# Optimization experiments

Hardware: AMD Instinct MI355X
Metric: run time of the kernel (lower is better)

Reference implementation:

```python
import jax, jax.numpy as jnp
import numpy as np

M, N, RANK = 4096, 4096, 64
LORA_ALPHA = 0.8
CODEBOOK_SCALE = 1.03  # E8P12 opt_scale; decompressed weights are divided by it


def fwht(x):
    """Normalized fast Walsh-Hadamard transform along the last axis (power-of-2 length).
    Matches matmul_hadU for power-of-2 dims (had_K is None, K=1)."""
    n = x.shape[-1]
    orig = x.shape
    x = x.reshape(-1, n)
    h = 1
    while h < n:
        x = x.reshape(-1, n // (2 * h), 2, h)
        a, b = x[:, :, 0, :], x[:, :, 1, :]
        x = jnp.stack([a + b, a - b], axis=2).reshape(-1, n)
        h *= 2
    return (x / jnp.sqrt(jnp.float32(n))).reshape(orig)


def decode_e8p(codes, grid):
    """E8P lattice codebook dequant (decompress_packed_e8p semantics).
    codes: int32 [M, N//8], one 16-bit codeword per 8-weight group.
    grid:  int32 [256] packed abs codebook; 8 nibbles per entry, nibble = 2*|w| in {1,3,5,7}.
    Bit layout: [0:8]=abs grid index, [8:15]=signs of first 7 coords,
    [15]=global +/-0.25 shift. 8th sign keeps the negative-sign count even."""
    abs_idx = codes & 0xFF
    sign_bits = (codes >> 8) & 0x7F
    shift_bit = (codes >> 15) & 1
    packed = grid[abs_idx]                                      # [M, N//8] int32
    nibs = (packed[..., None] >> (4 * jnp.arange(8))) & 0xF     # [M, N//8, 8]
    s7 = 1.0 - 2.0 * ((sign_bits[..., None] >> jnp.arange(7)) & 1).astype(jnp.float32)
    s8 = jnp.prod(s7, axis=-1, keepdims=True)                   # parity sign for 8th coord
    signs = jnp.concatenate([s7, s8], axis=-1)                  # [M, N//8, 8]
    delta = (2.0 * shift_bit.astype(jnp.float32) - 1.0)[..., None] * 0.25
    w = signs * (0.5 * nibs.astype(jnp.float32)) + delta
    return w.reshape(codes.shape[0], -1) / CODEBOOK_SCALE       # [M, N]


def build_W(Qidxs, grid, SU, SV, Wscale):
    W = decode_e8p(Qidxs, grid)   # [M, N]
    W = fwht(W)                   # Hadamard over in_features
    W = fwht(W.T).T               # Hadamard over out_features
    # per-channel sign/scale rescale; SV absorbs the global Wscale (SV *= Wscale)
    return W * (SV * Wscale)[:, None] * SU[None, :]


def setup_inputs() -> dict:
    key = jax.random.key(0)
    k1, k2, k3, k4, k5 = jax.random.split(key, 5)
    rng = np.random.default_rng(0)
    # packed abs codebook: 8 nibbles per int32, nibble = 2*|w| in {1,3,5,7}
    nibs = rng.integers(0, 4, size=(256, 8)).astype(np.int64) * 2 + 1
    grid = (nibs * (1 << (4 * np.arange(8)))).sum(axis=1).astype(np.int32)
    # one random 16-bit codeword per 8-weight group (int64 packing pre-split to int32)
    codes = rng.integers(0, 2 ** 16, size=(M, N // 8)).astype(np.int32)
    return {
        "input": jax.random.normal(k1, (1, 1024, N), dtype=jnp.float32),
        "SU": jnp.where(jax.random.uniform(k2, (N,)) < 0.5, -1.0, 1.0).astype(jnp.float32),
        "SV": jnp.where(jax.random.uniform(k3, (M,)) < 0.5, -1.0, 1.0).astype(jnp.float32),
        "Wscale": jnp.float32(0.02),
        "lora_A": jax.random.normal(k4, (M, RANK), dtype=jnp.float32) * 0.01,
        "lora_B": jax.random.normal(k5, (RANK, N), dtype=jnp.float32) * 0.01,
        "Qidxs": jnp.asarray(codes),
        "grid": jnp.asarray(grid),
    }


def reference(input, SU, SV, Wscale, lora_A, lora_B, Qidxs, grid):
    W = build_W(Qidxs, grid, SU, SV, Wscale)            # [M, N] dequantized weight
    out = jnp.einsum("bsn,mn->bsm", input, W)           # base quantized matmul
    lr = jnp.einsum("bsn,rn->bsr", input, lora_B)       # low-rank path
    out = out + LORA_ALPHA * jnp.einsum("bsr,mr->bsm", lr, lora_A)
    return out
```

## Files before the change

kernel.cpp:

```cpp
#include <hip/hip_runtime.h>
#include <hip/hip_bf16.h>

typedef unsigned short u16;
typedef float  floatx4 __attribute__((ext_vector_type(4)));
typedef short  bf16x8  __attribute__((ext_vector_type(8)));

#define GK 4352

__device__ __forceinline__ u16 f2bf_rne(float f) {
  union { float f; unsigned int u; } v; v.f = f;
  unsigned int r = v.u + 0x7FFFu + ((v.u >> 16) & 1u);
  return (u16)(r >> 16);
}
__device__ __forceinline__ float bf2f(u16 h) {
  union { unsigned int u; float f; } v; v.u = ((unsigned int)h) << 16;
  return v.f;
}

__device__ __forceinline__ void fwht4096_regs(float v[16], float* X, int w, int l) {
#pragma unroll
  for (int h = 1; h < 64; h <<= 1) {
#pragma unroll
    for (int k = 0; k < 16; ++k) {
      float o = __shfl_xor(v[k], h, 64);
      v[k] = (l & h) ? (o - v[k]) : (v[k] + o);
    }
  }
#pragma unroll
  for (int k = 0; k < 16; ++k) X[(w * 16 + k) * 64 + l] = v[k];
  __syncthreads();
  float s4 = (w & 1) ? -1.f : 1.f;
  float s5 = (w & 2) ? -1.f : 1.f;
#pragma unroll
  for (int k = 0; k < 16; ++k) {
    float x00 = X[(k     ) * 64 + l];
    float x01 = X[(k + 16) * 64 + l];
    float x10 = X[(k + 32) * 64 + l];
    float x11 = X[(k + 48) * 64 + l];
    v[k] = (x00 + s4 * x01) + s5 * (x10 + s4 * x11);
  }
#pragma unroll
  for (int h = 1; h < 16; h <<= 1) {
#pragma unroll
    for (int k = 0; k < 16; ++k) {
      if (!(k & h)) { float a = v[k], b = v[k ^ h]; v[k] = a + b; v[k ^ h] = a - b; }
    }
  }
}

__global__ __launch_bounds__(256) void prep_all_kernel(
    const float* __restrict__ x, const float* __restrict__ SU,
    const float* __restrict__ SV, const float* __restrict__ WscaleP,
    const float* __restrict__ loraA, const float* __restrict__ loraB,
    const int* __restrict__ codes, const int* __restrict__ grid,
    u16* __restrict__ Wd, u16* __restrict__ u, u16* __restrict__ Bh) {
  __shared__ float X[4096];
  int bid = blockIdx.x, t = threadIdx.x, l = t & 63, w = t >> 6;

  if (bid < 1024) {
    int s = bid;
    const float* xr = x + (size_t)s * 4096;
    float v[16];
#pragma unroll
    for (int k = 0; k < 16; ++k) {
      int i = (w * 16 + k) * 64 + l;
      v[k] = xr[i] * SU[i];
    }
    fwht4096_regs(v, X, w, l);
    __syncthreads();
    u16* Xu = (u16*)X;
#pragma unroll
    for (int k = 0; k < 16; ++k)
      Xu[(w * 16 + k) * 64 + l] = f2bf_rne(v[k] * 0.015625f);
    __syncthreads();
    u16* ur = u + (size_t)s * GK;
#pragma unroll
    for (int c = 0; c < 2; ++c) {
      int j = (t + 256 * c) * 8;
      *(uint4*)(ur + j) = *(const uint4*)(Xu + j);
    }
  } else if (bid < 1088) {
    int r = bid - 1024;
    float v[16];
#pragma unroll
    for (int k = 0; k < 16; ++k) {
      int i = (w * 16 + k) * 64 + l;
      v[k] = loraA[(size_t)i * 64 + r] * SV[i];
    }
    fwht4096_regs(v, X, w, l);
    float factor = (0.8f * 263.68f / 4096.0f) / WscaleP[0];
#pragma unroll
    for (int k = 0; k < 16; ++k) {
      int i = (w * 16 + k) * 64 + l;
      Wd[(size_t)i * GK + 4096 + r] = f2bf_rne(v[k] * factor);
    }
    {
      uint4 zv = make_uint4(0, 0, 0, 0);
#pragma unroll
      for (int j = 0; j < 6; ++j) {
        int idx = t + 256 * j;
        int row = idx / 24, cs = idx % 24;
        uint4* p = (uint4*)(Wd + (size_t)(r * 64 + row) * GK + 4160) + cs;
        *p = zv;
      }
    }
    __syncthreads();
#pragma unroll
    for (int k = 0; k < 16; ++k) {
      int i = (w * 16 + k) * 64 + l;
      v[k] = loraB[(size_t)r * 4096 + i] * SU[i];
    }
    fwht4096_regs(v, X, w, l);
#pragma unroll
    for (int k = 0; k < 16; ++k) {
      int i = (w * 16 + k) * 64 + l;
      Bh[(size_t)r * 4096 + i] = f2bf_rne(v[k] * 0.015625f);
    }
  } else {
    int* sgrid = (int*)X;
    sgrid[t] = grid[t & 255];
    __syncthreads();
    int idx = (bid - 1088) * 256 + t;
    int c = codes[idx];
    int abs_idx   = c & 255;
    int sign_bits = (c >> 8) & 127;
    int dlt       = 2 * ((c >> 15) & 1) - 1;
    int packed    = sgrid[abs_idx];
    int par       = __popc(sign_bits) & 1;
    u16 wv[8];
#pragma unroll
    for (int j = 0; j < 8; ++j) {
      int nib = (packed >> (4 * j)) & 15;
      int neg = (j < 7) ? ((sign_bits >> j) & 1) : par;
      int val = (neg ? -2 * nib : 2 * nib) + dlt;
      wv[j] = f2bf_rne((float)val);
    }
    uint4 pk;
    pk.x = (unsigned)wv[0] | ((unsigned)wv[1] << 16);
    pk.y = (unsigned)wv[2] | ((unsigned)wv[3] << 16);
    pk.z = (unsigned)wv[4] | ((unsigned)wv[5] << 16);
    pk.w = (unsigned)wv[6] | ((unsigned)wv[7] << 16);
    int m = idx >> 9, g = idx & 511;
    ((uint4*)Wd)[(size_t)m * (GK / 8) + g] = pk;
  }
}

__device__ __forceinline__ void stage128(const u16* __restrict__ src, int rowBase,
                                         int kt, char* ldsBase, int wg, int l) {
#pragma unroll
  for (int it = 0; it < 4; ++it) {
    int ci  = it * 4 + wg;
    int row = ci * 8 + (l >> 3);
    int cg  = (l & 7) ^ ((l >> 3) & 7);
    const u16* gp = src + (size_t)(rowBase + row) * GK + kt + cg * 8;
    __builtin_amdgcn_global_load_lds(
        (const __attribute__((address_space(1))) void*)gp,
        (__attribute__((address_space(3))) void*)(ldsBase + ci * 1024), 16, 0, 0);
  }
}
__device__ __forceinline__ void stage64n(const u16* __restrict__ src,
                                         int kt, char* ldsBase, int wg, int l) {
#pragma unroll
  for (int it = 0; it < 2; ++it) {
    int ci  = it * 4 + wg;
    int row = ci * 8 + (l >> 3);
    int cg  = (l & 7) ^ ((l >> 3) & 7);
    const u16* gp = src + (size_t)row * 4096 + kt + cg * 8;
    __builtin_amdgcn_global_load_lds(
        (const __attribute__((address_space(1))) void*)gp,
        (__attribute__((address_space(3))) void*)(ldsBase + ci * 1024), 16, 0, 0);
  }
}
__device__ __forceinline__ void stage_half(const u16* __restrict__ src, int rowBase,
                                           int kt, char* slotBase, int w, int l) {
#pragma unroll
  for (int it = 0; it < 2; ++it) {
    int ci  = it * 8 + w;
    int row = ci * 8 + (l >> 3);
    int cg  = (l & 7) ^ ((l >> 3) & 7);
    const u16* gp = src + (size_t)(rowBase + row) * GK + kt + cg * 8;
    __builtin_amdgcn_global_load_lds(
        (const __attribute__((address_space(1))) void*)gp,
        (__attribute__((address_space(3))) void*)(slotBase + ci * 1024), 16, 0, 0);
  }
}

__global__ __launch_bounds__(256) void lr_gemm_kernel(
    const u16* __restrict__ U,
    const u16* __restrict__ Bh,
    float* __restrict__ P) {
  __shared__ char lds[49152];
  int t = threadIdx.x, w = t >> 6, l = t & 63;
  int s0 = blockIdx.x * 128, k0 = blockIdx.y * 1024;
  int lr16 = l & 15, lk = l >> 4;
  char* ldsA = lds;
  char* ldsB = lds + 32768;

  floatx4 acc[2][4];
#pragma unroll
  for (int i = 0; i < 2; ++i)
#pragma unroll
    for (int j = 0; j < 4; ++j) acc[i][j] = (floatx4){0.f, 0.f, 0.f, 0.f};

  const int NT = 16;
  stage128(U,  s0, k0,      ldsA,         w, l);
  stage64n(Bh,     k0,      ldsB,         w, l);
  stage128(U,  s0, k0 + 64, ldsA + 16384, w, l);
  stage64n(Bh,     k0 + 64, ldsB + 8192,  w, l);
  asm volatile("s_waitcnt vmcnt(6)" ::: "memory");
  __builtin_amdgcn_s_barrier();

  for (int i = 0; i < NT; ++i) {
    int buf = i & 1;
    const char* sAc = ldsA + buf * 16384;
    const char* sBc = ldsB + buf * 8192;
    bf16x8 a[2][2], b[4][2];
#pragma unroll
    for (int ii = 0; ii < 2; ++ii)
#pragma unroll
      for (int ks = 0; ks < 2; ++ks) {
        int row = w * 32 + ii * 16 + lr16;
        int kb  = ks * 64 + lk * 16;
        a[ii][ks] = *(const bf16x8*)(sAc + (row << 7) + (kb ^ ((row & 7) << 4)));
      }
#pragma unroll
    for (int jj = 0; jj < 4; ++jj)
#pragma unroll
      for (int ks = 0; ks < 2; ++ks) {
        int row = jj * 16 + lr16;
        int kb  = ks * 64 + lk * 16;
        b[jj][ks] = *(const bf16x8*)(sBc + (row << 7) + (kb ^ ((row & 7) << 4)));
      }
    asm volatile("s_waitcnt lgkmcnt(0)" ::: "memory");
    __builtin_amdgcn_sched_barrier(0);
    bool do_stage = (i + 2) < NT;
    if (do_stage) {
      __builtin_amdgcn_s_barrier();
      stage128(U,  s0, k0 + (i + 2) * 64, ldsA + buf * 16384, w, l);
      stage64n(Bh,     k0 + (i + 2) * 64, ldsB + buf * 8192,  w, l);
    }
#pragma unroll
    for (int ks = 0; ks < 2; ++ks)
#pragma unroll
      for (int ii = 0; ii < 2; ++ii)
#pragma unroll
        for (int jj = 0; jj < 4; ++jj)
          acc[ii][jj] = __builtin_amdgcn_mfma_f32_16x16x32_bf16(
              a[ii][ks], b[jj][ks], acc[ii][jj], 0, 0, 0);
    if (i + 1 < NT) {
      if (do_stage) asm volatile("s_waitcnt vmcnt(6)" ::: "memory");
      else          asm volatile("s_waitcnt vmcnt(0)" ::: "memory");
      __builtin_amdgcn_s_barrier();
    }
  }
  float* Pb = P + (size_t)blockIdx.y * 65536;
#pragma unroll
  for (int ii = 0; ii < 2; ++ii)
#pragma unroll
    for (int jj = 0; jj < 4; ++jj) {
      int col  = jj * 16 + lr16;
      int rowb = s0 + w * 32 + ii * 16 + lk * 4;
#pragma unroll
      for (int q = 0; q < 4; ++q)
        Pb[(size_t)(rowb + q) * 64 + col] = acc[ii][jj][q];
    }
}

__global__ void lr_reduce_kernel(const float* __restrict__ P, u16* __restrict__ u) {
  int idx = blockIdx.x * 256 + threadIdx.x;
  float s = P[idx] + P[65536 + idx] + P[131072 + idx] + P[196608 + idx];
  int ss = idx >> 6, rr = idx & 63;
  u16* row = u + (size_t)ss * GK;
  row[4096 + rr] = f2bf_rne(s);
  row[4160 + rr] = 0;
  row[4224 + rr] = 0;
  row[4288 + rr] = 0;
}

__device__ __forceinline__ void rda(bf16x8 (&dst)[4][2], const char* base, int roff,
                                    int lr16, int lk) {
#pragma unroll
  for (int ii = 0; ii < 4; ++ii)
#pragma unroll
    for (int ks = 0; ks < 2; ++ks) {
      int r = roff + ii * 16 + lr16;
      dst[ii][ks] = *(const bf16x8*)(base + (r << 7) +
          ((ks * 64 + lk * 16) ^ ((r & 7) << 4)));
    }
}
__device__ __forceinline__ void rdb(bf16x8 (&dst)[2][2], const char* base, int roff,
                                    int lr16, int lk) {
#pragma unroll
  for (int jj = 0; jj < 2; ++jj)
#pragma unroll
    for (int ks = 0; ks < 2; ++ks) {
      int r = roff + jj * 16 + lr16;
      dst[jj][ks] = *(const bf16x8*)(base + (r << 7) +
          ((ks * 64 + lk * 16) ^ ((r & 7) << 4)));
    }
}
template<int IO, int JO>
__device__ __forceinline__ void mfq(const bf16x8 (&af)[4][2], const bf16x8 (&bf)[2][2],
                                    floatx4 (&acc)[8][4]) {
  __builtin_amdgcn_s_setprio(1);
#pragma unroll
  for (int ks = 0; ks < 2; ++ks)
#pragma unroll
    for (int ii = 0; ii < 4; ++ii)
#pragma unroll
      for (int jj = 0; jj < 2; ++jj)
        acc[IO + ii][JO + jj] = __builtin_amdgcn_mfma_f32_16x16x32_bf16(
            af[ii][ks], bf[jj][ks], acc[IO + ii][JO + jj], 0, 0, 0);
  __builtin_amdgcn_s_setprio(0);
}
#define PH_PRE()  do { __builtin_amdgcn_s_barrier(); \
                       asm volatile("s_waitcnt lgkmcnt(0)" ::: "memory"); } while (0)
#define PH_POST() __builtin_amdgcn_s_barrier()

__global__ __launch_bounds__(512, 2) void gemm_kernel(
    const u16* __restrict__ A,
    const u16* __restrict__ Bm,
    u16* __restrict__ zO,
    u16* __restrict__ zW) {
  __shared__ char lds[131072];
  int t = threadIdx.x, w = t >> 6, l = t & 63;
  int b = blockIdx.x;
  int xcd = b & 7, slot = b >> 3;
  int cell = slot >> 4, j4 = slot & 15;
  int x = (xcd & 3) * 4 + (j4 & 3);
  int g = (xcd >> 2) + 2 * cell;
  int y = j4 >> 2;
  int m0 = x * 256, s0 = y * 256;
  int wsd = w >> 2, wmd = w & 3;
  int lr16 = l & 15, lk = l >> 4;
  int boff = (wmd & 1) * 64;

  const char* A0b = lds + wsd * 16384;
  const char* B0b = lds + 32768 + (wmd >> 1) * 16384;
  const char* A1b = lds + 65536 + wsd * 16384;
  const char* B1b = lds + 98304 + (wmd >> 1) * 16384;

  floatx4 acc[8][4];
#pragma unroll
  for (int i = 0; i < 8; ++i)
#pragma unroll
    for (int jq = 0; jq < 4; ++jq) acc[i][jq] = (floatx4){0.f, 0.f, 0.f, 0.f};

  int kb0 = g * 1088;

  stage_half(A,  s0,       kb0,      lds +      0, w, l);
  stage_half(A,  s0 + 128, kb0,      lds +  16384, w, l);
  stage_half(Bm, m0,       kb0,      lds +  32768, w, l);
  stage_half(Bm, m0 + 128, kb0,      lds +  49152, w, l);
  stage_half(Bm, m0,       kb0 + 64, lds +  98304, w, l);
  stage_half(Bm, m0 + 128, kb0 + 64, lds + 114688, w, l);
  asm volatile("s_waitcnt vmcnt(4)" ::: "memory");
  __builtin_amdgcn_s_barrier();

  for (int j = 0; j < 8; ++j) {
    int kt1  = kb0 + (2 * j + 1) * 64;
    int ktn0 = kb0 + (2 * j + 2) * 64;
    int ktn1 = kb0 + (2 * j + 3) * 64;
    bf16x8 aF[4][2], aG[4][2], bF[2][2], bG[2][2];
    rda(aF, A0b, 0, lr16, lk); rdb(bF, B0b, boff, lr16, lk);
    stage_half(A, s0, kt1, lds + 65536, w, l);
    PH_PRE(); mfq<0, 0>(aF, bF, acc); PH_POST();
    rdb(bG, B0b, boff + 32, lr16, lk);
    stage_half(A, s0 + 128, kt1, lds + 81920, w, l);
    PH_PRE(); mfq<0, 2>(aF, bG, acc); PH_POST();
    rda(aG, A0b, 64, lr16, lk);
    stage_half(Bm, m0, ktn0, lds + 32768, w, l);
    PH_PRE(); mfq<4, 0>(aG, bF, acc); PH_POST();
    stage_half(Bm, m0 + 128, ktn0, lds + 49152, w, l);
    PH_PRE(); mfq<4, 2>(aG, bG, acc);
    asm volatile("s_waitcnt vmcnt(4)" ::: "memory");
    PH_POST();
    rda(aF, A1b, 0, lr16, lk); rdb(bF, B1b, boff, lr16, lk);
    stage_half(A, s0, ktn0, lds + 0, w, l);
    PH_PRE(); mfq<0, 0>(aF, bF, acc); PH_POST();
    rdb(bG, B1b, boff + 32, lr16, lk);
    stage_half(A, s0 + 128, ktn0, lds + 16384, w, l);
    PH_PRE(); mfq<0, 2>(aF, bG, acc); PH_POST();
    rda(aG, A1b, 64, lr16, lk);
    if (j < 7) stage_half(Bm, m0, ktn1, lds + 98304, w, l);
    PH_PRE(); mfq<4, 0>(aG, bF, acc); PH_POST();
    if (j < 7) stage_half(Bm, m0 + 128, ktn1, lds + 114688, w, l);
    PH_PRE(); mfq<4, 2>(aG, bG, acc);
    asm volatile("s_waitcnt vmcnt(4)" ::: "memory");
    PH_POST();
  }
  asm volatile("s_waitcnt vmcnt(0)" ::: "memory");
  __builtin_amdgcn_s_barrier();
  {
    bf16x8 aF[4][2], aG[4][2], bF[2][2], bG[2][2];
    rda(aF, A0b, 0, lr16, lk); rdb(bF, B0b, boff, lr16, lk);
    PH_PRE(); mfq<0, 0>(aF, bF, acc); PH_POST();
    rdb(bG, B0b, boff + 32, lr16, lk);
    PH_PRE(); mfq<0, 2>(aF, bG, acc); PH_POST();
    rda(aG, A0b, 64, lr16, lk);
    PH_PRE(); mfq<4, 0>(aG, bF, acc); PH_POST();
    PH_PRE(); mfq<4, 2>(aG, bG, acc);
  }
  u16* dst = (g < 2) ? zO : zW;
  int gg = g & 1;
#pragma unroll
  for (int ii = 0; ii < 8; ++ii)
#pragma unroll
    for (int jj = 0; jj < 4; ++jj) {
      int col  = m0 + wmd * 64 + jj * 16 + lr16;
      int rowb = s0 + wsd * 128 + ii * 16 + lk * 4;
#pragma unroll
      for (int q = 0; q < 4; ++q)
        dst[(size_t)(rowb + q) * 8192 + gg * 4096 + col] = f2bf_rne(acc[ii][jj][q]);
    }
}

__global__ __launch_bounds__(256) void final_kernel(const float* __restrict__ SV,
                                                    const float* __restrict__ WscaleP,
                                                    const u16* __restrict__ zW,
                                                    float* __restrict__ out) {
  __shared__ float X[4096];
  int s = blockIdx.x, t = threadIdx.x, l = t & 63, w = t >> 6;
  const u16* zr = (const u16*)out + (size_t)s * 8192;
  const u16* zw = zW + (size_t)s * 8192;
#pragma unroll
  for (int c = 0; c < 2; ++c) {
    int j = (t + 256 * c) * 8;
    uint4 a0 = *(const uint4*)(zr + j);
    uint4 a1 = *(const uint4*)(zr + 4096 + j);
    uint4 b0 = *(const uint4*)(zw + j);
    uint4 b1 = *(const uint4*)(zw + 4096 + j);
    const unsigned* pa0 = (const unsigned*)&a0;
    const unsigned* pa1 = (const unsigned*)&a1;
    const unsigned* pb0 = (const unsigned*)&b0;
    const unsigned* pb1 = (const unsigned*)&b1;
#pragma unroll
    for (int q = 0; q < 4; ++q) {
      X[j + 2 * q] = (bf2f((u16)pa0[q]) + bf2f((u16)pa1[q])) +
                     (bf2f((u16)pb0[q]) + bf2f((u16)pb1[q]));
      X[j + 2 * q + 1] = (bf2f((u16)(pa0[q] >> 16)) + bf2f((u16)(pa1[q] >> 16))) +
                         (bf2f((u16)(pb0[q] >> 16)) + bf2f((u16)(pb1[q] >> 16)));
    }
  }
  __syncthreads();
  float v[16];
#pragma unroll
  for (int k = 0; k < 16; ++k) v[k] = X[(w * 16 + k) * 64 + l];
  __syncthreads();
  fwht4096_regs(v, X, w, l);
  float gscale = WscaleP[0] * (1.0f / 263.68f);
  float* orow = out + (size_t)s * 4096;
#pragma unroll
  for (int k = 0; k < 16; ++k) {
    int i = (w * 16 + k) * 64 + l;
    orow[i] = v[k] * gscale * SV[i];
  }
}

extern "C" void kernel_launch(void* const* d_in, const int* in_sizes, int n_in,
                              void* d_out, int out_size, void* d_ws, size_t ws_size,
                              hipStream_t stream) {
  const float* x      = (const float*)d_in[0];
  const float* SU     = (const float*)d_in[1];
  const float* SV     = (const float*)d_in[2];
  const float* Wscale = (const float*)d_in[3];
  const float* loraA  = (const float*)d_in[4];
  const float* loraB  = (const float*)d_in[5];
  const int*   Qidxs  = (const int*)d_in[6];
  const int*   grid   = (const int*)d_in[7];
  float* out = (float*)d_out;

  char* ws = (char*)d_ws;
  u16* Wd = (u16*)ws;
  u16* u  = (u16*)(ws + 35651584);
  u16* Bh = (u16*)(ws + 35651584 + 8912896);
  float* P = (float*)(ws + 35651584 + 8912896 + 524288);
  u16* zW = (u16*)(ws + 35651584 + 8912896 + 524288 + 1048576);
  u16* zO = (u16*)out;

  prep_all_kernel<<<9280, 256, 0, stream>>>(x, SU, SV, Wscale, loraA, loraB,
                                            Qidxs, grid, Wd, u, Bh);
  dim3 lg(8, 4);
  lr_gemm_kernel<<<lg, 256, 0, stream>>>(u, Bh, P);
  lr_reduce_kernel<<<256, 256, 0, stream>>>(P, u);
  gemm_kernel<<<256, 512, 0, stream>>>(u, Wd, zO, zW);
  final_kernel<<<1024, 256, 0, stream>>>(SV, Wscale, zW, out);
}
```

Before: 80.56 us.

## Triple-buffer A tiles and restructure GEMM main loop into uniform 17-step pipeline

Restructures the GEMM K-loop from a double-buffered, manually unrolled two-stage body into a single loop over 17 K tiles. A tiles get three LDS buffers and B tiles get two, so A loads are issued three tiles ahead and B loads two tiles ahead. The intent is deeper prefetch that hides global-load latency behind the MFMA phases, with a looser vmcnt wait. In exchange LDS use per block grows to 160 KB, which likely limits the kernel to one block per CU despite launch bounds of 2 and reduces occupancy.

```diff
diff --git a/kernel.cpp b/kernel.cpp
--- a/kernel.cpp
+++ b/kernel.cpp
@@ -322,7 +322,7 @@
     const u16* __restrict__ Bm,
     u16* __restrict__ zO,
     u16* __restrict__ zW) {
-  __shared__ char lds[131072];
+  __shared__ char lds[163840];
   int t = threadIdx.x, w = t >> 6, l = t & 63;
   int b = blockIdx.x;
   int xcd = b & 7, slot = b >> 3;
@@ -335,10 +335,8 @@
   int lr16 = l & 15, lk = l >> 4;
   int boff = (wmd & 1) * 64;
 
-  const char* A0b = lds + wsd * 16384;
-  const char* B0b = lds + 32768 + (wmd >> 1) * 16384;
-  const char* A1b = lds + 65536 + wsd * 16384;
-  const char* B1b = lds + 98304 + (wmd >> 1) * 16384;
+  char* ldsA = lds;
+  char* ldsB = lds + 98304;
 
   floatx4 acc[8][4];
 #pragma unroll
@@ -348,59 +346,50 @@
 
   int kb0 = g * 1088;
 
-  stage_half(A,  s0,       kb0,      lds +      0, w, l);
-  stage_half(A,  s0 + 128, kb0,      lds +  16384, w, l);
-  stage_half(Bm, m0,       kb0,      lds +  32768, w, l);
-  stage_half(Bm, m0 + 128, kb0,      lds +  49152, w, l);
-  stage_half(Bm, m0,       kb0 + 64, lds +  98304, w, l);
-  stage_half(Bm, m0 + 128, kb0 + 64, lds + 114688, w, l);
-  asm volatile("s_waitcnt vmcnt(4)" ::: "memory");
+  stage_half(A,  s0,       kb0,       ldsA +     0, w, l);
+  stage_half(A,  s0 + 128, kb0,       ldsA + 16384, w, l);
+  stage_half(Bm, m0,       kb0,       ldsB +     0, w, l);
+  stage_half(Bm, m0 + 128, kb0,       ldsB + 16384, w, l);
+  stage_half(A,  s0,       kb0 + 64,  ldsA + 32768, w, l);
+  stage_half(A,  s0 + 128, kb0 + 64,  ldsA + 49152, w, l);
+  stage_half(Bm, m0,       kb0 + 64,  ldsB + 32768, w, l);
+  stage_half(Bm, m0 + 128, kb0 + 64,  ldsB + 49152, w, l);
+  stage_half(A,  s0,       kb0 + 128, ldsA + 65536, w, l);
+  stage_half(A,  s0 + 128, kb0 + 128, ldsA + 81920, w, l);
+  asm volatile("s_waitcnt vmcnt(12)" ::: "memory");
   __builtin_amdgcn_s_barrier();
 
-  for (int j = 0; j < 8; ++j) {
-    int kt1  = kb0 + (2 * j + 1) * 64;
-    int ktn0 = kb0 + (2 * j + 2) * 64;
-    int ktn1 = kb0 + (2 * j + 3) * 64;
+  int a3 = 0;
+  for (int tt = 0; tt < 17; ++tt) {
+    char* At = ldsA + a3 * 32768;
+    char* Bt = ldsB + (tt & 1) * 32768;
+    const char* Ar = At + wsd * 16384;
+    const char* Br = Bt + (wmd >> 1) * 16384;
     bf16x8 aF[4][2], aG[4][2], bF[2][2], bG[2][2];
-    rda(aF, A0b, 0, lr16, lk); rdb(bF, B0b, boff, lr16, lk);
-    stage_half(A, s0, kt1, lds + 65536, w, l);
+    rda(aF, Ar, 0, lr16, lk); rdb(bF, Br, boff, lr16, lk);
     PH_PRE(); mfq<0, 0>(aF, bF, acc); PH_POST();
-    rdb(bG, B0b, boff + 32, lr16, lk);
-    stage_half(A, s0 + 128, kt1, lds + 81920, w, l);
+    rda(aG, Ar, 64, lr16, lk);
+    PH_PRE(); mfq<4, 0>(aG, bF, acc); PH_POST();
+    rdb(bG, Br, boff + 32, lr16, lk);
+    if (tt + 3 <= 16) {
+      int kt3 = kb0 + (tt + 3) * 64;
+      stage_half(A, s0,       kt3, At,         w, l);
+      stage_half(A, s0 + 128, kt3, At + 16384, w, l);
+    }
     PH_PRE(); mfq<0, 2>(aF, bG, acc); PH_POST();
-    rda(aG, A0b, 64, lr16, lk);
-    stage_half(Bm, m0, ktn0, lds + 32768, w, l);
-    PH_PRE(); mfq<4, 0>(aG, bF, acc); PH_POST();
-    stage_half(Bm, m0 + 128, ktn0, lds + 49152, w, l);
+    if (tt + 2 <= 16) {
+      int kt2 = kb0 + (tt + 2) * 64;
+      stage_half(Bm, m0,       kt2, Bt,         w, l);
+      stage_half(Bm, m0 + 128, kt2, Bt + 16384, w, l);
+    }
     PH_PRE(); mfq<4, 2>(aG, bG, acc);
-    asm volatile("s_waitcnt vmcnt(4)" ::: "memory");
+    if (tt <= 13)      asm volatile("s_waitcnt vmcnt(8)" ::: "memory");
+    else if (tt == 14) asm volatile("s_waitcnt vmcnt(4)" ::: "memory");
+    else if (tt == 15) asm volatile("s_waitcnt vmcnt(0)" ::: "memory");
     PH_POST();
-    rda(aF, A1b, 0, lr16, lk); rdb(bF, B1b, boff, lr16, lk);
-    stage_half(A, s0, ktn0, lds + 0, w, l);
-    PH_PRE(); mfq<0, 0>(aF, bF, acc); PH_POST();
-    rdb(bG, B1b, boff + 32, lr16, lk);
-    stage_half(A, s0 + 128, ktn0, lds + 16384, w, l);
-    PH_PRE(); mfq<0, 2>(aF, bG, acc); PH_POST();
-    rda(aG, A1b, 64, lr16, lk);
-    if (j < 7) stage_half(Bm, m0, ktn1, lds + 98304, w, l);
-    PH_PRE(); mfq<4, 0>(aG, bF, acc); PH_POST();
-    if (j < 7) stage_half(Bm, m0 + 128, ktn1, lds + 114688, w, l);
-    PH_PRE(); mfq<4, 2>(aG, bG, acc);
-    asm volatile("s_waitcnt vmcnt(4)" ::: "memory");
-    PH_POST();
-  }
-  asm volatile("s_waitcnt vmcnt(0)" ::: "memory");
-  __builtin_amdgcn_s_barrier();
-  {
-    bf16x8 aF[4][2], aG[4][2], bF[2][2], bG[2][2];
-    rda(aF, A0b, 0, lr16, lk); rdb(bF, B0b, boff, lr16, lk);
-    PH_PRE(); mfq<0, 0>(aF, bF, acc); PH_POST();
-    rdb(bG, B0b, boff + 32, lr16, lk);
-    PH_PRE(); mfq<0, 2>(aF, bG, acc); PH_POST();
-    rda(aG, A0b, 64, lr16, lk);
-    PH_PRE(); mfq<4, 0>(aG, bF, acc); PH_POST();
-    PH_PRE(); mfq<4, 2>(aG, bG, acc);
-  }
+    a3 = (a3 == 2) ? 0 : a3 + 1;
+  }
+
   u16* dst = (g < 2) ? zO : zW;
   int gg = g & 1;
 #pragma unroll
```

Result: slower. 83.46 us (+3.6%).
